# Optimization experiments

Hardware: AMD Instinct MI355X
Metric: run time of the kernel (lower is better)

The kernel has to match this reference:

```python
import jax, jax.numpy as jnp
import numpy as np

H = 1024
EPS = 1e-5
N_ENT = 1000
TOP_K = 5


def _ln(x, g, b):
    mu = jnp.mean(x, axis=-1, keepdims=True)
    var = jnp.mean((x - mu) ** 2, axis=-1, keepdims=True)
    return (x - mu) * jax.lax.rsqrt(var + EPS) * g + b


def _gelu(x):
    return jax.nn.gelu(x, approximate=False)  # torch nn.GELU default (erf)


def setup_inputs() -> dict:
    key = jax.random.key(0)
    ks = jax.random.split(key, 24)
    s = 0.02
    inp = {
        'hidden_states': jax.random.normal(ks[0], (8, 2048, H), jnp.float32),
        'entity_embeddings': jax.random.normal(ks[1], (N_ENT, H), jnp.float32) * 0.01,
        # entity_encoder: H -> 2H -> H -> LN
        'ee_w1': jax.random.normal(ks[2], (H, 2 * H), jnp.float32) * s,
        'ee_b1': jnp.zeros((2 * H,), jnp.float32),
        'ee_w2': jax.random.normal(ks[3], (2 * H, H), jnp.float32) * s,
        'ee_b2': jnp.zeros((H,), jnp.float32),
        'ee_g': jnp.ones((H,), jnp.float32),
        'ee_beta': jnp.zeros((H,), jnp.float32),
        # relation_encoder: H -> H -> H -> LN
        're_w1': jax.random.normal(ks[4], (H, H), jnp.float32) * s,
        're_b1': jnp.zeros((H,), jnp.float32),
        're_w2': jax.random.normal(ks[5], (H, H), jnp.float32) * s,
        're_b2': jnp.zeros((H,), jnp.float32),
        're_g': jnp.ones((H,), jnp.float32),
        're_beta': jnp.zeros((H,), jnp.float32),
        # reasoning_network: 3H -> 2H -> H -> LN
        'rn_w1': jax.random.normal(ks[6], (3 * H, 2 * H), jnp.float32) * s,
        'rn_b1': jnp.zeros((2 * H,), jnp.float32),
        'rn_w2': jax.random.normal(ks[7], (2 * H, H), jnp.float32) * s,
        'rn_b2': jnp.zeros((H,), jnp.float32),
        'rn_g': jnp.ones((H,), jnp.float32),
        'rn_beta': jnp.zeros((H,), jnp.float32),
        # validation_network: H -> H/2 -> 1 -> sigmoid
        'vn_w1': jax.random.normal(ks[8], (H, H // 2), jnp.float32) * s,
        'vn_b1': jnp.zeros((H // 2,), jnp.float32),
        'vn_w2': jax.random.normal(ks[9], (H // 2, 1), jnp.float32) * s,
        'vn_b2': jnp.zeros((1,), jnp.float32),
    }
    return inp


def reference(hidden_states, entity_embeddings,
              ee_w1, ee_b1, ee_w2, ee_b2, ee_g, ee_beta,
              re_w1, re_b1, re_w2, re_b2, re_g, re_beta,
              rn_w1, rn_b1, rn_w2, rn_b2, rn_g, rn_beta,
              vn_w1, vn_b1, vn_w2, vn_b2):
    # entity encoder over all tokens: [B,S,H]
    entity_features = _ln(_gelu(hidden_states @ ee_w1 + ee_b1) @ ee_w2 + ee_b2, ee_g, ee_beta)

    # query=None path: relation encoder on mean-pooled hidden states [B,H]
    pooled = jnp.mean(hidden_states, axis=1)
    relation_features = _ln(_gelu(pooled @ re_w1 + re_b1) @ re_w2 + re_b2, re_g, re_beta)
    query_features = relation_features

    # similarity + top-k entity retrieval
    entity_similarities = query_features @ entity_embeddings.T  # [B, N_ENT]
    top_values, top_indices = jax.lax.top_k(entity_similarities, TOP_K)
    retrieved_entities = entity_embeddings[top_indices]  # [B, K, H]

    # reasoning input: [mean retrieved entity | relation | mean context]
    entity_vec = jnp.mean(retrieved_entities, axis=1)  # [B,H]
    context_vec = jnp.mean(hidden_states, axis=1)      # [B,H]
    reasoning_in = jnp.concatenate([entity_vec, relation_features, context_vec], axis=-1)  # [B,3H]
    reasoning_output = _ln(_gelu(reasoning_in @ rn_w1 + rn_b1) @ rn_w2 + rn_b2, rn_g, rn_beta)

    validation_scores = jax.nn.sigmoid(_gelu(reasoning_output @ vn_w1 + vn_b1) @ vn_w2 + vn_b2)

    return (entity_features, relation_features, retrieved_entities,
            entity_similarities, top_indices, reasoning_output, validation_scores)
```

## Files before the change

### kernel.cpp

```cpp
#include <hip/hip_runtime.h>
#include <math.h>

#define H 1024
#define SEQ 2048
#define BATCH 8
#define N_ENT 1000
#define TOPK 5
#define LN_EPS 1e-5f

using bf16x8 = __attribute__((ext_vector_type(8))) __bf16;
using f32x4  = __attribute__((ext_vector_type(4))) float;
#define AS1 __attribute__((address_space(1)))
#define AS3 __attribute__((address_space(3)))


__device__ __forceinline__ float gelu_fast(float x) {
    float z = fabsf(x) * 0.70710678118654752440f;
    float t = __builtin_amdgcn_rcpf(fmaf(0.3275911f, z, 1.0f));
    float p = fmaf(fmaf(fmaf(fmaf(1.061405429f, t, -1.453152027f), t, 1.421413741f),
                        t, -0.284496736f), t, 0.254829592f) * t;
    float e = __builtin_amdgcn_exp2f(-z * z * 1.44269504088896f);
    float erfz = fmaf(-p, e, 1.0f);
    float s = copysignf(erfz, x);
    return 0.5f * x * (1.0f + s);
}

__device__ __forceinline__ float sigmoidf_(float x) {
    return 1.0f / (1.0f + expf(-x));
}

__device__ __forceinline__ unsigned short f2bf(float f) {
    unsigned int u = __float_as_uint(f);
    unsigned int r = (u + 0x7fffu + ((u >> 16) & 1u)) >> 16;
    return (unsigned short)r;
}

__device__ float block_sum(float v, float* red) {
    for (int off = 32; off > 0; off >>= 1) v += __shfl_down(v, off, 64);
    int wid = threadIdx.x >> 6;
    int lane = threadIdx.x & 63;
    int nw = blockDim.x >> 6;
    if (lane == 0) red[wid] = v;
    __syncthreads();
    if (threadIdx.x == 0) {
        float s = 0.f;
        for (int i = 0; i < nw; ++i) s += red[i];
        red[0] = s;
    }
    __syncthreads();
    float r = red[0];
    __syncthreads();
    return r;
}


__global__ void f2bf_kernel(const float* __restrict__ in, unsigned short* __restrict__ out, int n) {
    int i = (blockIdx.x * blockDim.x + threadIdx.x) * 4;
    if (i >= n) return;
    float4 v = *(const float4*)(in + i);
    ushort4 o;
    o.x = f2bf(v.x); o.y = f2bf(v.y); o.z = f2bf(v.z); o.w = f2bf(v.w);
    *(ushort4*)(out + i) = o;
}

__global__ void transpose_bf_kernel(const float* __restrict__ in, unsigned short* __restrict__ out,
                                    int R, int C) {
    __shared__ float tile[32][33];
    int c0 = blockIdx.x * 32, r0 = blockIdx.y * 32;
    int tx = threadIdx.x & 31, ty = threadIdx.x >> 5;
#pragma unroll
    for (int i = 0; i < 32; i += 8)
        tile[ty + i][tx] = in[(size_t)(r0 + ty + i) * C + c0 + tx];
    __syncthreads();
#pragma unroll
    for (int i = 0; i < 32; i += 8)
        out[(size_t)(c0 + ty + i) * R + r0 + tx] = f2bf(tile[tx][ty + i]);
}


__global__ void pool1_kernel(const float* __restrict__ hs, float* __restrict__ part,
                             unsigned short* __restrict__ hsb) {
    int sc = blockIdx.x, b = blockIdx.y, t = threadIdx.x;
    size_t rowbase = (size_t)b * SEQ + sc * 64;
    const float* p = hs + rowbase * H + t * 4;
    float4 a = {0.f, 0.f, 0.f, 0.f};
    for (int s = 0; s < 64; ++s) {
        float4 v = *(const float4*)(p + (size_t)s * H);
        a.x += v.x; a.y += v.y; a.z += v.z; a.w += v.w;
        if (hsb) {
            ushort4 o;
            o.x = f2bf(v.x); o.y = f2bf(v.y); o.z = f2bf(v.z); o.w = f2bf(v.w);
            *(ushort4*)(hsb + (rowbase + s) * H + t * 4) = o;
        }
    }
    *(float4*)(part + ((size_t)b * 32 + sc) * H + t * 4) = a;
}

__global__ void pool2_kernel(const float* __restrict__ part, float* __restrict__ pooled) {
    int b = blockIdx.x, t = threadIdx.x;
    float4 s = {0.f, 0.f, 0.f, 0.f};
    for (int sc = 0; sc < 32; ++sc) {
        float4 v = *(const float4*)(part + ((size_t)b * 32 + sc) * H + t * 4);
        s.x += v.x; s.y += v.y; s.z += v.z; s.w += v.w;
    }
    float4 o = {s.x * (1.0f / SEQ), s.y * (1.0f / SEQ), s.z * (1.0f / SEQ), s.w * (1.0f / SEQ)};
    *(float4*)(pooled + (size_t)b * H + t * 4) = o;
}


template <int KRANGE>
__global__ void mlp_partial_kernel(const float* __restrict__ X, int ldx,
                                   const float* __restrict__ W, int N,
                                   float* __restrict__ part) {
    __shared__ float xs[8][KRANGE];
    int jb = blockIdx.x, ks = blockIdx.y, t = threadIdx.x;
    int k0 = ks * KRANGE;
    for (int i = t; i < 8 * KRANGE; i += 256) {
        int b = i / KRANGE, k = i % KRANGE;
        xs[b][k] = X[(size_t)b * ldx + k0 + k];
    }
    __syncthreads();
    int j = jb * 256 + t;
    float acc[8] = {};
    for (int k = 0; k < KRANGE; ++k) {
        float w = W[(size_t)(k0 + k) * N + j];
#pragma unroll
        for (int b = 0; b < 8; ++b) acc[b] = fmaf(xs[b][k], w, acc[b]);
    }
#pragma unroll
    for (int b = 0; b < 8; ++b) part[((size_t)ks * 8 + b) * N + j] = acc[b];
}

__global__ void mlp_reduce_gelu_kernel(const float* __restrict__ part, const float* __restrict__ bias,
                                       float* __restrict__ out, int N, int nks) {
    int b = blockIdx.y;
    int j = blockIdx.x * 256 + threadIdx.x;
    float s = bias[j];
    for (int ks = 0; ks < nks; ++ks) s += part[((size_t)ks * 8 + b) * N + j];
    out[(size_t)b * N + j] = gelu_fast(s);
}

__global__ void mlp_reduce_ln_kernel(const float* __restrict__ part, const float* __restrict__ bias,
                                     const float* __restrict__ g, const float* __restrict__ be,
                                     float* __restrict__ out, int nks) {
    __shared__ float red[32];
    int b = blockIdx.x, t = threadIdx.x;
    float s = bias[t];
    for (int ks = 0; ks < nks; ++ks) s += part[((size_t)ks * 8 + b) * H + t];
    float mu = block_sum(s, red) * (1.0f / H);
    float d = s - mu;
    float var = block_sum(d * d, red) * (1.0f / H);
    out[(size_t)b * H + t] = d * rsqrtf(var + LN_EPS) * g[t] + be[t];
}


__global__ void sim_kernel(const float* __restrict__ rel, const float* __restrict__ ent,
                           float* __restrict__ sims) {
    __shared__ float rl[8 * H];
    int t = threadIdx.x;
    for (int i = t; i < 8 * H; i += 256) rl[i] = rel[i];
    __syncthreads();
    int e = blockIdx.x * 4 + (t >> 6);
    int lane = t & 63;
    float ev[16];
    const float* ep = ent + (size_t)e * H;
#pragma unroll
    for (int i = 0; i < 16; ++i) ev[i] = ep[lane + i * 64];
#pragma unroll
    for (int b = 0; b < 8; ++b) {
        float a = 0.f;
#pragma unroll
        for (int i = 0; i < 16; ++i) a = fmaf(ev[i], rl[b * H + lane + i * 64], a);
        for (int off = 32; off > 0; off >>= 1) a += __shfl_down(a, off, 64);
        if (lane == 0) sims[b * N_ENT + e] = a;
    }
}

__global__ void topk_kernel(const float* __restrict__ sims, float* __restrict__ out_idx_f,
                            int* __restrict__ idx_i) {
    __shared__ float v[1024];
    __shared__ float rv[4];
    __shared__ int ri[4];
    int b = blockIdx.x, t = threadIdx.x;
    for (int i = t; i < 1024; i += 256) v[i] = (i < N_ENT) ? sims[b * N_ENT + i] : -INFINITY;
    __syncthreads();
    for (int k = 0; k < TOPK; ++k) {
        float best = -INFINITY;
        int bi = 0x7fffffff;
        for (int i = t; i < 1024; i += 256) {
            float x = v[i];
            if (x > best || (x == best && i < bi)) { best = x; bi = i; }
        }
        for (int off = 32; off > 0; off >>= 1) {
            float ov = __shfl_down(best, off, 64);
            int oi = __shfl_down(bi, off, 64);
            if (ov > best || (ov == best && oi < bi)) { best = ov; bi = oi; }
        }
        if ((t & 63) == 0) { rv[t >> 6] = best; ri[t >> 6] = bi; }
        __syncthreads();
        if (t == 0) {
            for (int w = 1; w < 4; ++w)
                if (rv[w] > rv[0] || (rv[w] == rv[0] && ri[w] < ri[0])) { rv[0] = rv[w]; ri[0] = ri[w]; }
            int sel = ri[0];
            out_idx_f[b * TOPK + k] = (float)sel;
            idx_i[b * TOPK + k] = sel;
            v[sel] = -INFINITY;
        }
        __syncthreads();
    }
}

__global__ void gather_concat_kernel(const float* __restrict__ ent, const int* __restrict__ idx,
                                     const float* __restrict__ rel, const float* __restrict__ pooled,
                                     float* __restrict__ retrieved, float* __restrict__ xin) {
    int b = blockIdx.x, h = threadIdx.x;
    float acc = 0.f;
    for (int k = 0; k < TOPK; ++k) {
        float v = ent[(size_t)idx[b * TOPK + k] * H + h];
        retrieved[((size_t)b * TOPK + k) * H + h] = v;
        acc += v;
    }
    float* xb = xin + (size_t)b * 3 * H;
    xb[h] = acc * (1.0f / TOPK);
    xb[H + h] = rel[b * H + h];
    xb[2 * H + h] = pooled[b * H + h];
}

__global__ void vn_final_kernel(const float* __restrict__ part, const float* __restrict__ b1,
                                const float* __restrict__ w2, const float* __restrict__ b2,
                                float* __restrict__ vs, int nks) {
    __shared__ float red[32];
    int b = blockIdx.x, t = threadIdx.x;
    float s = b1[t];
    for (int ks = 0; ks < nks; ++ks) s += part[((size_t)ks * 8 + b) * 512 + t];
    float c = gelu_fast(s) * w2[t];
    float tot = block_sum(c, red);
    if (t == 0) vs[b] = sigmoidf_(tot + b2[0]);
}

template <int GELU_BF16_OUT>
__global__ __launch_bounds__(512, 2) void gemm256_8ph(const unsigned short* __restrict__ A,
                                                      const unsigned short* __restrict__ Bt,
                                                      const float* __restrict__ bias,
                                                      void* __restrict__ Cout,
                                                      int M, int N, int K) {
    __shared__ __align__(16) unsigned short As[4][128 * 64];
    __shared__ __align__(16) unsigned short Bs[4][128 * 64];
    const int tid = threadIdx.x;
    const int lane = tid & 63;
    const int w = tid >> 6;
    const int wm2 = w >> 2;
    const int wn4 = w & 3;

    const int Np = N >> 8;
    const int nwg = gridDim.x;
    int bid = blockIdx.x;
    int s = bid;
    if ((nwg & 7) == 0) s = (bid & 7) * (nwg >> 3) + (bid >> 3);
    const int m0 = (s / Np) << 8;
    const int n0 = (s % Np) << 8;

    const int nT = K >> 6;

    const int l7 = lane & 7;
    const int lrow0 = w * 16 + (lane >> 3);
    const int lrow1 = lrow0 + 8;
    const int kel0 = ((l7 ^ (lrow0 & 7)) << 3);
    const int kel1 = ((l7 ^ (lrow1 & 7)) << 3);
    const unsigned short* pa0 = A + (size_t)(m0 + lrow0) * K + kel0;
    const unsigned short* pa1 = A + (size_t)(m0 + lrow1) * K + kel1;
    const unsigned short* pb0 = Bt + (size_t)(n0 + lrow0) * K + kel0;
    const unsigned short* pb1 = Bt + (size_t)(n0 + lrow1) * K + kel1;
    const size_t halfstep = (size_t)128 * K;
    const int dst0 = (w * 16) * 64;
    const int dst1 = dst0 + 8 * 64;

    auto stageA = [&](int t, int half) {
        if (t >= nT) return;
        int slot = (2 * t + half) & 3;
        int koff = t << 6;
        __builtin_amdgcn_global_load_lds((AS1 void*)(pa0 + half * halfstep + koff),
                                         (AS3 void*)(&As[slot][dst0]), 16, 0, 0);
        __builtin_amdgcn_global_load_lds((AS1 void*)(pa1 + half * halfstep + koff),
                                         (AS3 void*)(&As[slot][dst1]), 16, 0, 0);
    };
    auto stageB = [&](int t, int half) {
        if (t >= nT) return;
        int slot = (2 * t + half) & 3;
        int koff = t << 6;
        __builtin_amdgcn_global_load_lds((AS1 void*)(pb0 + half * halfstep + koff),
                                         (AS3 void*)(&Bs[slot][dst0]), 16, 0, 0);
        __builtin_amdgcn_global_load_lds((AS1 void*)(pb1 + half * halfstep + koff),
                                         (AS3 void*)(&Bs[slot][dst1]), 16, 0, 0);
    };

    const int arow = lane & 15;
    const int xk0 = (((lane >> 4) << 4)) ^ (l7 << 4);
    const int xk1 = (64 + ((lane >> 4) << 4)) ^ (l7 << 4);
    auto ldf = [&](const unsigned short* slotbase, int rowbase, int xk) -> bf16x8 {
        return *(const bf16x8*)((const char*)slotbase + (rowbase + arow) * 128 + xk);
    };

    f32x4 acc[8][4] = {};

    stageA(0, 0); stageA(0, 1); stageB(0, 0); stageB(0, 1);
    asm volatile("s_waitcnt vmcnt(4)" ::: "memory");
    stageA(1, 0); stageB(1, 0); stageB(1, 1);
    asm volatile("s_waitcnt vmcnt(6)" ::: "memory");
    __builtin_amdgcn_s_barrier();

    bf16x8 af0[4][2], af1[4][2], bf0[2][2], bf1[2][2];

    for (int T = 0; T < nT; ++T) {
        const unsigned short* Aslot0 = As[(2 * T) & 3];
        const unsigned short* Aslot1 = As[(2 * T + 1) & 3];
        const unsigned short* Bslot0 = Bs[(2 * T) & 3];
        const unsigned short* Bslot1 = Bs[(2 * T + 1) & 3];

#pragma unroll
        for (int ii = 0; ii < 4; ++ii) {
            af0[ii][0] = ldf(Aslot0, ii * 32 + wm2 * 16, xk0);
            af0[ii][1] = ldf(Aslot0, ii * 32 + wm2 * 16, xk1);
        }
#pragma unroll
        for (int jj = 0; jj < 2; ++jj) {
            bf0[jj][0] = ldf(Bslot0, jj * 64 + wn4 * 16, xk0);
            bf0[jj][1] = ldf(Bslot0, jj * 64 + wn4 * 16, xk1);
        }
        stageA(T + 1, 1);
        __builtin_amdgcn_s_barrier();
        __builtin_amdgcn_s_setprio(1);
#pragma unroll
        for (int ii = 0; ii < 4; ++ii)
#pragma unroll
            for (int jj = 0; jj < 2; ++jj) {
                acc[ii][jj] = __builtin_amdgcn_mfma_f32_16x16x32_bf16(af0[ii][0], bf0[jj][0], acc[ii][jj], 0, 0, 0);
                acc[ii][jj] = __builtin_amdgcn_mfma_f32_16x16x32_bf16(af0[ii][1], bf0[jj][1], acc[ii][jj], 0, 0, 0);
            }
        __builtin_amdgcn_s_setprio(0);
        __builtin_amdgcn_s_barrier();

#pragma unroll
        for (int jj = 0; jj < 2; ++jj) {
            bf1[jj][0] = ldf(Bslot1, jj * 64 + wn4 * 16, xk0);
            bf1[jj][1] = ldf(Bslot1, jj * 64 + wn4 * 16, xk1);
        }
        stageA(T + 2, 0);
        __builtin_amdgcn_s_barrier();
        __builtin_amdgcn_s_setprio(1);
#pragma unroll
        for (int ii = 0; ii < 4; ++ii)
#pragma unroll
            for (int jj = 0; jj < 2; ++jj) {
                acc[ii][2 + jj] = __builtin_amdgcn_mfma_f32_16x16x32_bf16(af0[ii][0], bf1[jj][0], acc[ii][2 + jj], 0, 0, 0);
                acc[ii][2 + jj] = __builtin_amdgcn_mfma_f32_16x16x32_bf16(af0[ii][1], bf1[jj][1], acc[ii][2 + jj], 0, 0, 0);
            }
        __builtin_amdgcn_s_setprio(0);
        __builtin_amdgcn_s_barrier();

#pragma unroll
        for (int ii = 0; ii < 4; ++ii) {
            af1[ii][0] = ldf(Aslot1, ii * 32 + wm2 * 16, xk0);
            af1[ii][1] = ldf(Aslot1, ii * 32 + wm2 * 16, xk1);
        }
        stageB(T + 2, 0);
        __builtin_amdgcn_s_barrier();
        __builtin_amdgcn_s_setprio(1);
#pragma unroll
        for (int ii = 0; ii < 4; ++ii)
#pragma unroll
            for (int jj = 0; jj < 2; ++jj) {
                acc[4 + ii][jj] = __builtin_amdgcn_mfma_f32_16x16x32_bf16(af1[ii][0], bf0[jj][0], acc[4 + ii][jj], 0, 0, 0);
                acc[4 + ii][jj] = __builtin_amdgcn_mfma_f32_16x16x32_bf16(af1[ii][1], bf0[jj][1], acc[4 + ii][jj], 0, 0, 0);
            }
        __builtin_amdgcn_s_setprio(0);
        __builtin_amdgcn_s_barrier();

        stageB(T + 2, 1);
        if (T + 3 <= nT) {
            asm volatile("s_waitcnt vmcnt(6)" ::: "memory");
        } else {
            asm volatile("s_waitcnt vmcnt(0)" ::: "memory");
        }
        __builtin_amdgcn_s_barrier();
        __builtin_amdgcn_s_setprio(1);
#pragma unroll
        for (int ii = 0; ii < 4; ++ii)
#pragma unroll
            for (int jj = 0; jj < 2; ++jj) {
                acc[4 + ii][2 + jj] = __builtin_amdgcn_mfma_f32_16x16x32_bf16(af1[ii][0], bf1[jj][0], acc[4 + ii][2 + jj], 0, 0, 0);
                acc[4 + ii][2 + jj] = __builtin_amdgcn_mfma_f32_16x16x32_bf16(af1[ii][1], bf1[jj][1], acc[4 + ii][2 + jj], 0, 0, 0);
            }
        __builtin_amdgcn_s_setprio(0);
        __builtin_amdgcn_s_barrier();
    }

    const int cn = lane & 15;
    const int rbase = (lane >> 4) * 4;
#pragma unroll
    for (int i = 0; i < 8; ++i) {
        int mbase = m0 + (i >> 2) * 128 + (i & 3) * 32 + wm2 * 16 + rbase;
#pragma unroll
        for (int j = 0; j < 4; ++j) {
            int n = n0 + (j >> 1) * 128 + (j & 1) * 64 + wn4 * 16 + cn;
            float bv = bias[n];
#pragma unroll
            for (int r = 0; r < 4; ++r) {
                float c = acc[i][j][r] + bv;
                if (GELU_BF16_OUT) {
                    c = gelu_fast(c);
                    ((unsigned short*)Cout)[(size_t)(mbase + r) * N + n] = f2bf(c);
                } else {
                    ((float*)Cout)[(size_t)(mbase + r) * N + n] = c;
                }
            }
        }
    }
}

__global__ void ln_rows_kernel(float* __restrict__ x, const float* __restrict__ g,
                               const float* __restrict__ beta) {
    __shared__ float red[32];
    float* p = x + (size_t)blockIdx.x * H;
    int t = threadIdx.x;
    float4 v = *(const float4*)(p + t * 4);
    float s = v.x + v.y + v.z + v.w;
    float mu = block_sum(s, red) * (1.0f / H);
    float4 d = { v.x - mu, v.y - mu, v.z - mu, v.w - mu };
    float d2 = d.x * d.x + d.y * d.y + d.z * d.z + d.w * d.w;
    float var = block_sum(d2, red) * (1.0f / H);
    float inv = rsqrtf(var + LN_EPS);
    float4 gg = *(const float4*)(g + t * 4);
    float4 bb = *(const float4*)(beta + t * 4);
    float4 o = { d.x * inv * gg.x + bb.x, d.y * inv * gg.y + bb.y,
                 d.z * inv * gg.z + bb.z, d.w * inv * gg.w + bb.w };
    *(float4*)(p + t * 4) = o;
}


extern "C" void kernel_launch(void* const* d_in, const int* in_sizes, int n_in,
                              void* d_out, int out_size, void* d_ws, size_t ws_size,
                              hipStream_t stream) {
    const float* hs     = (const float*)d_in[0];
    const float* ent    = (const float*)d_in[1];
    const float* ee_w1  = (const float*)d_in[2];
    const float* ee_b1  = (const float*)d_in[3];
    const float* ee_w2  = (const float*)d_in[4];
    const float* ee_b2  = (const float*)d_in[5];
    const float* ee_g   = (const float*)d_in[6];
    const float* ee_be  = (const float*)d_in[7];
    const float* re_w1  = (const float*)d_in[8];
    const float* re_b1  = (const float*)d_in[9];
    const float* re_w2  = (const float*)d_in[10];
    const float* re_b2  = (const float*)d_in[11];
    const float* re_g   = (const float*)d_in[12];
    const float* re_be  = (const float*)d_in[13];
    const float* rn_w1  = (const float*)d_in[14];
    const float* rn_b1  = (const float*)d_in[15];
    const float* rn_w2  = (const float*)d_in[16];
    const float* rn_b2  = (const float*)d_in[17];
    const float* rn_g   = (const float*)d_in[18];
    const float* rn_be  = (const float*)d_in[19];
    const float* vn_w1  = (const float*)d_in[20];
    const float* vn_b1  = (const float*)d_in[21];
    const float* vn_w2  = (const float*)d_in[22];
    const float* vn_b2  = (const float*)d_in[23];

    float* out = (float*)d_out;
    float* ef   = out;
    float* rel  = ef + (size_t)BATCH * SEQ * H;
    float* retr = rel + BATCH * H;
    float* sims = retr + BATCH * TOPK * H;
    float* tidx = sims + BATCH * N_ENT;
    float* ro   = tidx + BATCH * TOPK;
    float* vs   = ro + BATCH * H;

    float* ws = (float*)d_ws;
    size_t o = 0;
    float* pooled = ws + o; o += 8192;
    int*   idx_i  = (int*)(ws + o); o += 64;
    float* xin    = ws + o; o += 8 * 3 * H;
    float* h1r    = ws + o; o += 8 * H;
    float* h1n    = ws + o; o += 8 * 2 * H;
    float* part   = ws + o; o += 24 * 8 * 2048;
    unsigned short* w1t = (unsigned short*)(ws + o); o += (2048 * 1024) / 2;
    unsigned short* w2t = (unsigned short*)(ws + o); o += (2048 * 1024) / 2;
    unsigned short* hsb = (unsigned short*)(ws + o);

    long long avail = (long long)(ws_size / 4) - (long long)o;
    int chunk = (int)(avail / 1536);
    chunk &= ~255;
    int total = BATCH * SEQ;
    if (chunk > total) chunk = total;
    if (chunk < 256) chunk = 256;
    bool full = (chunk >= total);
    unsigned short* midb = hsb + (size_t)chunk * H;

    transpose_bf_kernel<<<dim3(2048 / 32, 1024 / 32), 256, 0, stream>>>(ee_w1, w1t, 1024, 2048);
    transpose_bf_kernel<<<dim3(1024 / 32, 2048 / 32), 256, 0, stream>>>(ee_w2, w2t, 2048, 1024);

    pool1_kernel<<<dim3(32, BATCH), 256, 0, stream>>>(hs, part, full ? hsb : nullptr);
    pool2_kernel<<<BATCH, 256, 0, stream>>>(part, pooled);

    mlp_partial_kernel<64><<<dim3(4, 16), 256, 0, stream>>>(pooled, H, re_w1, H, part);
    mlp_reduce_gelu_kernel<<<dim3(4, 8), 256, 0, stream>>>(part, re_b1, h1r, H, 16);
    mlp_partial_kernel<64><<<dim3(4, 16), 256, 0, stream>>>(h1r, H, re_w2, H, part);
    mlp_reduce_ln_kernel<<<BATCH, 1024, 0, stream>>>(part, re_b2, re_g, re_be, rel, 16);

    sim_kernel<<<250, 256, 0, stream>>>(rel, ent, sims);
    topk_kernel<<<BATCH, 256, 0, stream>>>(sims, tidx, idx_i);
    gather_concat_kernel<<<BATCH, 1024, 0, stream>>>(ent, idx_i, rel, pooled, retr, xin);

    mlp_partial_kernel<128><<<dim3(8, 24), 256, 0, stream>>>(xin, 3 * H, rn_w1, 2 * H, part);
    mlp_reduce_gelu_kernel<<<dim3(8, 8), 256, 0, stream>>>(part, rn_b1, h1n, 2 * H, 24);
    mlp_partial_kernel<128><<<dim3(4, 16), 256, 0, stream>>>(h1n, 2 * H, rn_w2, H, part);
    mlp_reduce_ln_kernel<<<BATCH, 1024, 0, stream>>>(part, rn_b2, rn_g, rn_be, ro, 16);

    mlp_partial_kernel<128><<<dim3(2, 8), 256, 0, stream>>>(ro, H, vn_w1, 512, part);
    vn_final_kernel<<<BATCH, 512, 0, stream>>>(part, vn_b1, vn_w2, vn_b2, vs, 8);

    for (int r0 = 0; r0 < total; r0 += chunk) {
        int m = total - r0;
        if (m > chunk) m = chunk;
        if (!full) {
            int nconv = m * H;
            f2bf_kernel<<<(nconv / 4 + 255) / 256, 256, 0, stream>>>(hs + (size_t)r0 * H, hsb, nconv);
        }
        unsigned short* a1 = full ? (hsb + (size_t)r0 * H) : hsb;
        gemm256_8ph<1><<<(m / 256) * (2048 / 256), 512, 0, stream>>>(a1, w1t, ee_b1, midb,
                                                                     m, 2048, 1024);
        gemm256_8ph<0><<<(m / 256) * (1024 / 256), 512, 0, stream>>>(midb, w2t, ee_b2,
                                                                     ef + (size_t)r0 * H,
                                                                     m, 1024, 2048);
    }
    ln_rows_kernel<<<total, 256, 0, stream>>>(ef, ee_g, ee_be);
}
```

Baseline: 537.1 us.

## Stage GEMM epilogue through LDS, fuse small-MLP reduce+GELU, merge transposes

The big GEMM epilogue now writes results into swizzled shared memory and then emits coalesced 16-byte row stores, replacing scattered per-element global stores. The small MLP chain drops its separate reduce+GELU kernels by folding the partial-sum reduction into the next layer's input staging, and uses finer K splits for more blocks. The two weight transposes are merged into one launch. These changes aim to cut launch count and improve store coalescing, at the cost of redundant partial-sum reads per block and extra barriers in the epilogue.

```diff
diff --git a/kernel.cpp b/kernel.cpp
--- a/kernel.cpp
+++ b/kernel.cpp
@@ -63,10 +63,14 @@
     *(ushort4*)(out + i) = o;
 }
 
-__global__ void transpose_bf_kernel(const float* __restrict__ in, unsigned short* __restrict__ out,
-                                    int R, int C) {
+__global__ void transpose_both_kernel(const float* __restrict__ w1, unsigned short* __restrict__ o1,
+                                      const float* __restrict__ w2, unsigned short* __restrict__ o2) {
     __shared__ float tile[32][33];
-    int c0 = blockIdx.x * 32, r0 = blockIdx.y * 32;
+    int bid = blockIdx.x;
+    const float* in; unsigned short* out; int R, C, bx, by;
+    if (bid < 2048) { in = w1; out = o1; R = 1024; C = 2048; bx = bid & 63; by = bid >> 6; }
+    else { bid -= 2048; in = w2; out = o2; R = 2048; C = 1024; bx = bid & 31; by = bid >> 5; }
+    int c0 = bx * 32, r0 = by * 32;
     int tx = threadIdx.x & 31, ty = threadIdx.x >> 5;
 #pragma unroll
     for (int i = 0; i < 32; i += 8)
@@ -128,16 +132,34 @@
         for (int b = 0; b < 8; ++b) acc[b] = fmaf(xs[b][k], w, acc[b]);
     }
 #pragma unroll
-    for (int b = 0; b < 8; ++b) part[((size_t)ks * 8 + b) * N + j] = acc[b];
-}
-
-__global__ void mlp_reduce_gelu_kernel(const float* __restrict__ part, const float* __restrict__ bias,
-                                       float* __restrict__ out, int N, int nks) {
-    int b = blockIdx.y;
-    int j = blockIdx.x * 256 + threadIdx.x;
-    float s = bias[j];
-    for (int ks = 0; ks < nks; ++ks) s += part[((size_t)ks * 8 + b) * N + j];
-    out[(size_t)b * N + j] = gelu_fast(s);
+    for (int b = 0; b < 8; ++b) part[((size_t)(ks * 8 + b)) * N + j] = acc[b];
+}
+
+template <int KRANGE>
+__global__ void mlp_partial_fused_kernel(const float* __restrict__ Pprev, int ldp, int nksp,
+                                         const float* __restrict__ b1,
+                                         const float* __restrict__ W, int N,
+                                         float* __restrict__ part) {
+    __shared__ float xs[8][KRANGE];
+    int jb = blockIdx.x, ks = blockIdx.y, t = threadIdx.x;
+    int k0 = ks * KRANGE;
+    for (int i = t; i < 8 * KRANGE; i += 256) {
+        int b = i / KRANGE, k = i % KRANGE;
+        int col = k0 + k;
+        float s = b1[col];
+        for (int q = 0; q < nksp; ++q) s += Pprev[((size_t)(q * 8 + b)) * ldp + col];
+        xs[b][k] = gelu_fast(s);
+    }
+    __syncthreads();
+    int j = jb * 256 + t;
+    float acc[8] = {};
+    for (int k = 0; k < KRANGE; ++k) {
+        float w = W[(size_t)(k0 + k) * N + j];
+#pragma unroll
+        for (int b = 0; b < 8; ++b) acc[b] = fmaf(xs[b][k], w, acc[b]);
+    }
+#pragma unroll
+    for (int b = 0; b < 8; ++b) part[((size_t)(ks * 8 + b)) * N + j] = acc[b];
 }
 
 __global__ void mlp_reduce_ln_kernel(const float* __restrict__ part, const float* __restrict__ bias,
@@ -146,7 +168,7 @@
     __shared__ float red[32];
     int b = blockIdx.x, t = threadIdx.x;
     float s = bias[t];
-    for (int ks = 0; ks < nks; ++ks) s += part[((size_t)ks * 8 + b) * H + t];
+    for (int ks = 0; ks < nks; ++ks) s += part[((size_t)(ks * 8 + b)) * H + t];
     float mu = block_sum(s, red) * (1.0f / H);
     float d = s - mu;
     float var = block_sum(d * d, red) * (1.0f / H);
@@ -232,7 +254,7 @@
     __shared__ float red[32];
     int b = blockIdx.x, t = threadIdx.x;
     float s = b1[t];
-    for (int ks = 0; ks < nks; ++ks) s += part[((size_t)ks * 8 + b) * 512 + t];
+    for (int ks = 0; ks < nks; ++ks) s += part[((size_t)(ks * 8 + b)) * 512 + t];
     float c = gelu_fast(s) * w2[t];
     float tot = block_sum(c, red);
     if (t == 0) vs[b] = sigmoidf_(tot + b2[0]);
@@ -244,8 +266,9 @@
                                                       const float* __restrict__ bias,
                                                       void* __restrict__ Cout,
                                                       int M, int N, int K) {
-    __shared__ __align__(16) unsigned short As[4][128 * 64];
-    __shared__ __align__(16) unsigned short Bs[4][128 * 64];
+    __shared__ __align__(16) unsigned short smem[65536];
+    unsigned short (*As)[8192] = (unsigned short(*)[8192])smem;
+    unsigned short (*Bs)[8192] = (unsigned short(*)[8192])(smem + 32768);
     const int tid = threadIdx.x;
     const int lane = tid & 63;
     const int w = tid >> 6;
@@ -397,22 +420,65 @@
 
     const int cn = lane & 15;
     const int rbase = (lane >> 4) * 4;
-#pragma unroll
-    for (int i = 0; i < 8; ++i) {
-        int mbase = m0 + (i >> 2) * 128 + (i & 3) * 32 + wm2 * 16 + rbase;
-#pragma unroll
-        for (int j = 0; j < 4; ++j) {
-            int n = n0 + (j >> 1) * 128 + (j & 1) * 64 + wn4 * 16 + cn;
-            float bv = bias[n];
-#pragma unroll
-            for (int r = 0; r < 4; ++r) {
-                float c = acc[i][j][r] + bv;
-                if (GELU_BF16_OUT) {
-                    c = gelu_fast(c);
-                    ((unsigned short*)Cout)[(size_t)(mbase + r) * N + n] = f2bf(c);
-                } else {
-                    ((float*)Cout)[(size_t)(mbase + r) * N + n] = c;
+    __syncthreads();
+
+    if (GELU_BF16_OUT) {
+#pragma unroll
+        for (int i = 0; i < 8; ++i) {
+            int lr = (i >> 2) * 128 + (i & 3) * 32 + wm2 * 16 + rbase;
+#pragma unroll
+            for (int j = 0; j < 4; ++j) {
+                int nl = (j >> 1) * 128 + (j & 1) * 64 + wn4 * 16 + cn;
+                float bv = bias[n0 + nl];
+#pragma unroll
+                for (int r = 0; r < 4; ++r) {
+                    float c = gelu_fast(acc[i][j][r] + bv);
+                    int row = lr + r;
+                    int byte = (row << 9) + (nl << 1);
+                    byte ^= (row & 7) << 4;
+                    *(unsigned short*)((char*)smem + byte) = f2bf(c);
                 }
+            }
+        }
+        __syncthreads();
+#pragma unroll
+        for (int u = 0; u < 16; ++u) {
+            int off = u * 8192 + tid * 16;
+            int row = off >> 9, colb = off & 511;
+            int src = off ^ ((row & 7) << 4);
+            *(int4*)((char*)Cout + ((size_t)(m0 + row) * N + n0) * 2 + colb) =
+                *(const int4*)((const char*)smem + src);
+        }
+    } else {
+        float* smf = (float*)smem;
+#pragma unroll
+        for (int p = 0; p < 2; ++p) {
+            if (p) __syncthreads();
+#pragma unroll
+            for (int ii = 0; ii < 4; ++ii) {
+                int i = p * 4 + ii;
+                int lr = (i & 3) * 32 + wm2 * 16 + rbase;
+#pragma unroll
+                for (int j = 0; j < 4; ++j) {
+                    int nl = (j >> 1) * 128 + (j & 1) * 64 + wn4 * 16 + cn;
+                    float bv = bias[n0 + nl];
+#pragma unroll
+                    for (int r = 0; r < 4; ++r) {
+                        int row = lr + r;
+                        int byte = (row << 10) + (nl << 2);
+                        byte ^= (row & 7) << 4;
+                        *(float*)((char*)smf + byte) = acc[p * 4 + ii][j][r] + bv;
+                    }
+                }
+            }
+            __syncthreads();
+#pragma unroll
+            for (int u = 0; u < 16; ++u) {
+                int off = u * 8192 + tid * 16;
+                int row = off >> 10, colb = off & 1023;
+                int src = off ^ ((row & 7) << 4);
+                *(int4*)((char*)Cout + ((size_t)(m0 + p * 128 + row) * N + n0) * 4 + colb) =
+                    *(const int4*)((const char*)smf + src);
             }
         }
     }
@@ -480,9 +546,8 @@
     float* pooled = ws + o; o += 8192;
     int*   idx_i  = (int*)(ws + o); o += 64;
     float* xin    = ws + o; o += 8 * 3 * H;
-    float* h1r    = ws + o; o += 8 * H;
-    float* h1n    = ws + o; o += 8 * 2 * H;
-    float* part   = ws + o; o += 24 * 8 * 2048;
+    float* partA  = ws + o; o += 48 * 8 * 2048;
+    float* partB  = ws + o; o += 32 * 8 * 1024;
     unsigned short* w1t = (unsigned short*)(ws + o); o += (2048 * 1024) / 2;
     unsigned short* w2t = (unsigned short*)(ws + o); o += (2048 * 1024) / 2;
     unsigned short* hsb = (unsigned short*)(ws + o);
@@ -496,28 +561,28 @@
     bool full = (chunk >= total);
     unsigned short* midb = hsb + (size_t)chunk * H;
 
-    transpose_bf_kernel<<<dim3(2048 / 32, 1024 / 32), 256, 0, stream>>>(ee_w1, w1t, 1024, 2048);
-    transpose_bf_kernel<<<dim3(1024 / 32, 2048 / 32), 256, 0, stream>>>(ee_w2, w2t, 2048, 1024);
-
-    pool1_kernel<<<dim3(32, BATCH), 256, 0, stream>>>(hs, part, full ? hsb : nullptr);
-    pool2_kernel<<<BATCH, 256, 0, stream>>>(part, pooled);
-
-    mlp_partial_kernel<64><<<dim3(4, 16), 256, 0, stream>>>(pooled, H, re_w1, H, part);
-    mlp_reduce_gelu_kernel<<<dim3(4, 8), 256, 0, stream>>>(part, re_b1, h1r, H, 16);
-    mlp_partial_kernel<64><<<dim3(4, 16), 256, 0, stream>>>(h1r, H, re_w2, H, part);
-    mlp_reduce_ln_kernel<<<BATCH, 1024, 0, stream>>>(part, re_b2, re_g, re_be, rel, 16);
+    pool1_kernel<<<dim3(32, BATCH), 256, 0, stream>>>(hs, partA, full ? hsb : nullptr);
+
+    transpose_both_kernel<<<4096, 256, 0, stream>>>(ee_w1, w1t, ee_w2, w2t);
+
+    pool2_kernel<<<BATCH, 256, 0, stream>>>(partA, pooled);
+
+    mlp_partial_kernel<32><<<dim3(4, 32), 256, 0, stream>>>(pooled, H, re_w1, H, partA);
+    mlp_partial_fused_kernel<32><<<dim3(4, 32), 256, 0, stream>>>(partA, H, 32, re_b1,
+                                                                  re_w2, H, partB);
+    mlp_reduce_ln_kernel<<<BATCH, 1024, 0, stream>>>(partB, re_b2, re_g, re_be, rel, 32);
 
     sim_kernel<<<250, 256, 0, stream>>>(rel, ent, sims);
     topk_kernel<<<BATCH, 256, 0, stream>>>(sims, tidx, idx_i);
     gather_concat_kernel<<<BATCH, 1024, 0, stream>>>(ent, idx_i, rel, pooled, retr, xin);
 
-    mlp_partial_kernel<128><<<dim3(8, 24), 256, 0, stream>>>(xin, 3 * H, rn_w1, 2 * H, part);
-    mlp_reduce_gelu_kernel<<<dim3(8, 8), 256, 0, stream>>>(part, rn_b1, h1n, 2 * H, 24);
-    mlp_partial_kernel<128><<<dim3(4, 16), 256, 0, stream>>>(h1n, 2 * H, rn_w2, H, part);
-    mlp_reduce_ln_kernel<<<BATCH, 1024, 0, stream>>>(part, rn_b2, rn_g, rn_be, ro, 16);
-
-    mlp_partial_kernel<128><<<dim3(2, 8), 256, 0, stream>>>(ro, H, vn_w1, 512, part);
-    vn_final_kernel<<<BATCH, 512, 0, stream>>>(part, vn_b1, vn_w2, vn_b2, vs, 8);
+    mlp_partial_kernel<64><<<dim3(8, 48), 256, 0, stream>>>(xin, 3 * H, rn_w1, 2 * H, partA);
+    mlp_partial_fused_kernel<64><<<dim3(4, 32), 256, 0, stream>>>(partA, 2 * H, 48, rn_b1,
+                                                                  rn_w2, H, partB);
+    mlp_reduce_ln_kernel<<<BATCH, 1024, 0, stream>>>(partB, rn_b2, rn_g, rn_be, ro, 32);
+
+    mlp_partial_kernel<64><<<dim3(2, 16), 256, 0, stream>>>(ro, H, vn_w1, 512, partA);
+    vn_final_kernel<<<BATCH, 512, 0, stream>>>(partA, vn_b1, vn_w2, vn_b2, vs, 16);
 
     for (int r0 = 0; r0 < total; r0 += chunk) {
         int m = total - r0;
```

Measured after the change: 534.5 us. About the same (-0.5%).
